# Performance work log

Measured on AMD Instinct MI355X. Metric: run time of the kernel, lower is better.

The kernel has to match this reference:

```python
import jax, jax.numpy as jnp
import numpy as np

E = 512   # embed_size
H = 8     # heads
D = E // H
WIN = 256 # window_size
N = 4     # batch
S = 2048  # seq len (query_len == key_len == value_len)


def setup_inputs() -> dict:
    key = jax.random.key(0)
    ks = jax.random.split(key, 8)
    s = 0.02
    inp = {
        "value": jax.random.normal(ks[0], (N, S, E), jnp.float32),
        "key":   jax.random.normal(ks[1], (N, S, E), jnp.float32),
        "query": jax.random.normal(ks[2], (N, S, E), jnp.float32),
        "mask":  jnp.ones((N, 1, 1, S), jnp.int32),
        # nn.Linear params: y = x @ W.T + b, W shape [out, in]
        "Wv": jax.random.normal(ks[3], (E, E), jnp.float32) * s,
        "bv": jnp.zeros((E,), jnp.float32),
        "Wk": jax.random.normal(ks[4], (E, E), jnp.float32) * s,
        "bk": jnp.zeros((E,), jnp.float32),
        "Wq": jax.random.normal(ks[5], (E, E), jnp.float32) * s,
        "bq": jnp.zeros((E,), jnp.float32),
        "Wo": jax.random.normal(ks[6], (E, E), jnp.float32) * s,
        "bo": jnp.zeros((E,), jnp.float32),
    }
    return inp


def reference(value, key, query, mask, Wv, bv, Wk, bk, Wq, bq, Wo, bo):
    n, q_len, _ = query.shape
    k_len = key.shape[1]
    w = min(WIN, k_len)  # window_size = min(self.window_size, key_len)

    v = (value @ Wv.T + bv).reshape(n, k_len, H, D)
    k = (key   @ Wk.T + bk).reshape(n, k_len, H, D)
    q = (query @ Wq.T + bq).reshape(n, q_len, H, D)

    # Full QK scores; banded window selected below. Position j is inside the
    # window of query i iff  i - w//2 <= j <= i + w//2 (matches the torch
    # per-i slice [max(0,i-w//2), min(k_len, i+w//2+1)) ).
    scores = jnp.einsum('nqhd,nkhd->nhqk', q, k)  # [N,H,Q,K]
    ii = jnp.arange(q_len)[:, None]
    jj = jnp.arange(k_len)[None, :]
    in_win = (jj >= ii - w // 2) & (jj <= ii + w // 2)  # [Q,K]

    # Inside window: scores, masked to -inf where mask == 0.
    # Outside window: entries stay 0 (the torch code zero-inits attention).
    neg_inf = jnp.float32(-jnp.inf)
    banded = jnp.where(mask != 0, scores, neg_inf)          # broadcast [N,1,1,K]
    att_logits = jnp.where(in_win[None, None], banded, 0.0)  # [N,H,Q,K]

    att_logits = att_logits / jnp.sqrt(jnp.float32(E))  # scale by sqrt(embed_size)
    attention = jax.nn.softmax(att_logits, axis=3)

    out = jnp.einsum('nhqk,nkhd->nqhd', attention, v).reshape(n, q_len, E)
    out = out @ Wo.T + bo
    return (out, attention)
```

## Files before the change

### kernel.cpp

```cpp
#include <hip/hip_runtime.h>


typedef unsigned short u16;
typedef __bf16 bf16x8 __attribute__((ext_vector_type(8)));
typedef float  f32x4  __attribute__((ext_vector_type(4)));
typedef u16    u16x8  __attribute__((ext_vector_type(8)));

#define GLOAD_LDS(gsrc, ldst)                                                  \
    __builtin_amdgcn_global_load_lds(                                          \
        (const __attribute__((address_space(1))) void*)(gsrc),                 \
        (__attribute__((address_space(3))) void*)(ldst), 16, 0, 0)

__device__ __forceinline__ u16 f2bf(float f) {
    union { float f; unsigned u; } x; x.f = f;
    unsigned u = x.u;
    u += 0x7fffu + ((u >> 16) & 1u);
    return (u16)(u >> 16);
}
__device__ __forceinline__ int swzc(int c, int r) {
    return (c < 32) ? (c ^ (r & 7)) : c;
}

struct CvtArgs {
    const float* src[7];
    u16*         dst[7];
};

__global__ __launch_bounds__(256) void cvt_kernel(CvtArgs a) {
    int bid = blockIdx.x;
    int t, blk;
    if (bid < 12288) { t = bid >> 12; blk = bid & 4095; }
    else { int r = bid - 12288; t = 3 + (r >> 8); blk = r & 255; }
    int i = (blk * 256 + threadIdx.x) * 4;
    float4 v = *(const float4*)(a.src[t] + i);
    ushort4 o;
    o.x = f2bf(v.x); o.y = f2bf(v.y); o.z = f2bf(v.z); o.w = f2bf(v.w);
    *(ushort4*)(a.dst[t] + i) = o;
}

__global__ __launch_bounds__(256) void gemm_qkv(
    const u16* __restrict__ A0, const u16* __restrict__ A1, const u16* __restrict__ A2,
    const u16* __restrict__ B,
    const float* __restrict__ b0, const float* __restrict__ b1, const float* __restrict__ b2,
    u16* __restrict__ o0, u16* __restrict__ o1, u16* __restrict__ o2,
    float* __restrict__ sumv)
{
    __shared__ __attribute__((aligned(16))) u16 As[128 * 64];
    __shared__ __attribute__((aligned(16))) u16 Bs[128 * 64];

    const int tid  = threadIdx.x;
    const int lane = tid & 63;
    const int w    = tid >> 6;
    const int bm   = blockIdx.x, bn = blockIdx.y;
    const int wm   = w >> 1, wn = w & 1;

    const int t = bn >> 2;
    const u16* A = (t == 0) ? A0 : (t == 1) ? A1 : A2;
    const u16* Ag = A + (size_t)bm * 128 * 512;
    const u16* Bg = B + (size_t)bn * 128 * 512;

    f32x4 acc[4][4];
#pragma unroll
    for (int m = 0; m < 4; ++m)
#pragma unroll
        for (int n = 0; n < 4; ++n) acc[m][n] = 0;

    const int swc = ((lane & 7) ^ (lane >> 3)) * 8;

    for (int k0 = 0; k0 < 512; k0 += 64) {
#pragma unroll
        for (int i = 0; i < 4; ++i) {
            int g = i * 4 + w;
            int row = g * 8 + (lane >> 3);
            GLOAD_LDS(Ag + (size_t)row * 512 + k0 + swc, As + g * 512);
            GLOAD_LDS(Bg + (size_t)row * 512 + k0 + swc, Bs + g * 512);
        }
        __syncthreads();

#pragma unroll
        for (int s = 0; s < 2; ++s) {
            bf16x8 af[4], bf[4];
            int c = s * 4 + (lane >> 4);
#pragma unroll
            for (int m = 0; m < 4; ++m) {
                int r = wm * 64 + m * 16 + (lane & 15);
                af[m] = *(const bf16x8*)(As + r * 64 + ((c ^ (r & 7)) * 8));
                int r2 = wn * 64 + m * 16 + (lane & 15);
                bf[m] = *(const bf16x8*)(Bs + r2 * 64 + ((c ^ (r2 & 7)) * 8));
            }
#pragma unroll
            for (int m = 0; m < 4; ++m)
#pragma unroll
                for (int n = 0; n < 4; ++n)
                    acc[m][n] = __builtin_amdgcn_mfma_f32_16x16x32_bf16(af[m], bf[n], acc[m][n], 0, 0, 0);
        }
        __syncthreads();
    }

    const float* bias = (t == 0) ? b0 : (t == 1) ? b1 : b2;
    u16* ob = (t == 0) ? o0 : (t == 1) ? o1 : o2;
    const int clbase = (bn & 3) * 128;

#pragma unroll
    for (int m = 0; m < 4; ++m) {
#pragma unroll
        for (int n = 0; n < 4; ++n) {
            int cl = clbase + wn * 64 + n * 16 + (lane & 15);
            float bb = bias[cl];
#pragma unroll
            for (int reg = 0; reg < 4; ++reg) {
                int row = bm * 128 + wm * 64 + m * 16 + (lane >> 4) * 4 + reg;
                ob[(size_t)row * 512 + cl] = f2bf(acc[m][n][reg] + bb);
            }
        }
    }

    if (t == 2) {
        int nb = bm >> 4;
#pragma unroll
        for (int n = 0; n < 4; ++n) {
            float s = 0.f;
#pragma unroll
            for (int m = 0; m < 4; ++m)
#pragma unroll
                for (int reg = 0; reg < 4; ++reg) s += acc[m][n][reg];
            s += __shfl_xor(s, 16, 64);
            s += __shfl_xor(s, 32, 64);
            if (lane < 16) {
                int cl = clbase + wn * 64 + n * 16 + lane;
                atomicAdd(sumv + nb * 512 + cl, s);
            }
        }
    }
}

__global__ __launch_bounds__(256) void gemm_o(
    const u16* __restrict__ A, const u16* __restrict__ B,
    const float* __restrict__ bias, float* __restrict__ fo)
{
    __shared__ __attribute__((aligned(16))) u16 As[128 * 64];
    __shared__ __attribute__((aligned(16))) u16 Bs[64 * 64];

    const int tid  = threadIdx.x;
    const int lane = tid & 63;
    const int w    = tid >> 6;
    const int bm   = blockIdx.x, bn = blockIdx.y;
    const int wm   = w >> 1, wn = w & 1;

    const u16* Ag = A + (size_t)bm * 128 * 512;
    const u16* Bg = B + (size_t)bn * 64 * 512;

    f32x4 acc[4][2];
#pragma unroll
    for (int m = 0; m < 4; ++m) { acc[m][0] = 0; acc[m][1] = 0; }

    const int swc = ((lane & 7) ^ (lane >> 3)) * 8;

    for (int k0 = 0; k0 < 512; k0 += 64) {
#pragma unroll
        for (int i = 0; i < 4; ++i) {
            int g = i * 4 + w;
            GLOAD_LDS(Ag + (size_t)(g * 8 + (lane >> 3)) * 512 + k0 + swc, As + g * 512);
        }
#pragma unroll
        for (int i = 0; i < 2; ++i) {
            int g = i * 4 + w;
            GLOAD_LDS(Bg + (size_t)(g * 8 + (lane >> 3)) * 512 + k0 + swc, Bs + g * 512);
        }
        __syncthreads();

#pragma unroll
        for (int s = 0; s < 2; ++s) {
            bf16x8 af[4], bf[2];
            int c = s * 4 + (lane >> 4);
#pragma unroll
            for (int m = 0; m < 4; ++m) {
                int r = wm * 64 + m * 16 + (lane & 15);
                af[m] = *(const bf16x8*)(As + r * 64 + ((c ^ (r & 7)) * 8));
            }
#pragma unroll
            for (int n = 0; n < 2; ++n) {
                int r2 = wn * 32 + n * 16 + (lane & 15);
                bf[n] = *(const bf16x8*)(Bs + r2 * 64 + ((c ^ (r2 & 7)) * 8));
            }
#pragma unroll
            for (int m = 0; m < 4; ++m)
#pragma unroll
                for (int n = 0; n < 2; ++n)
                    acc[m][n] = __builtin_amdgcn_mfma_f32_16x16x32_bf16(af[m], bf[n], acc[m][n], 0, 0, 0);
        }
        __syncthreads();
    }

#pragma unroll
    for (int m = 0; m < 4; ++m) {
#pragma unroll
        for (int n = 0; n < 2; ++n) {
            int cl = bn * 64 + wn * 32 + n * 16 + (lane & 15);
            float bb = bias[cl];
#pragma unroll
            for (int reg = 0; reg < 4; ++reg) {
                int row = bm * 128 + wm * 64 + m * 16 + (lane >> 4) * 4 + reg;
                fo[(size_t)row * 512 + cl] = acc[m][n][reg] + bb;
            }
        }
    }
}

__global__ __launch_bounds__(256) void attn_kernel(
    const u16* __restrict__ qb, const u16* __restrict__ kb,
    const u16* __restrict__ vb, const int* __restrict__ mask,
    const float* __restrict__ sumv, float* __restrict__ att,
    u16* __restrict__ oh, float* __restrict__ c_buf) {
    __shared__ __attribute__((aligned(16))) char lds[78848];
    u16*   Qs      = (u16*)lds;
    float* stat_m  = (float*)lds;
    float* stat_rd = (float*)(lds + 128);
    float* stat_c  = (float*)(lds + 256);
    float* red     = (float*)(lds + 384);
    float* red2    = (float*)(lds + 640);
    u16*   Ks      = (u16*)(lds + 4096);
    u16*   Ab      = Ks;
    u16*   Vt      = (u16*)(lds + 4096 + 36864);

    const int tid  = threadIdx.x;
    const int lane = tid & 63;
    const int w    = tid >> 6;
    const int bid0 = blockIdx.x;
    const int bid  = (bid0 & 7) * 256 + (bid0 >> 3);
    const int tile = bid & 63;
    const int h    = (bid >> 6) & 7;
    const int n    = bid >> 9;
    const int i0   = tile * 32;
    const int jlo  = max(0, i0 - 128);
    const float scale = 0.04419417382415922f;

    const size_t base_nh = (size_t)n * 2048 * 512 + h * 64;
    const int lr = lane >> 3;
    const int swg = ((lane & 7) ^ lr) * 8;

    GLOAD_LDS(qb + base_nh + (size_t)(i0 + w * 8 + lr) * 512 + swg, Qs + w * 512);
    for (int p = 0; p < 9; ++p) {
        int g = p * 4 + w;
        int j = min(jlo + g * 8 + lr, 2047);
        GLOAD_LDS(kb + base_nh + (size_t)j * 512 + swg, Ks + g * 512);
    }
    for (int p = 0; p < 9; ++p) {
        int idx = p * 256 + tid;
        int jj = idx >> 3, ch = idx & 7;
        int j = jlo + jj;
        u16x8 tmp = {0, 0, 0, 0, 0, 0, 0, 0};
        if (j < 2048) tmp = *(const u16x8*)(vb + base_nh + (size_t)j * 512 + ch * 8);
        int jc = jj >> 3, jr = jj & 7;
        int pjc = (jc < 32) ? (jc ^ ch) : jc;
#pragma unroll
        for (int r = 0; r < 8; ++r)
            Vt[(ch * 8 + r) * 296 + pjc * 8 + jr] = tmp[r];
    }
    __syncthreads();

    const int rbase = (w & 1) * 16;
    const int cbase = (w >> 1) * 144;
    f32x4 acc[9];
#pragma unroll
    for (int f = 0; f < 9; ++f) acc[f] = 0;

    bf16x8 aq[2];
    {
        int r = rbase + (lane & 15);
#pragma unroll
        for (int ks = 0; ks < 2; ++ks) {
            int kc = ks * 4 + (lane >> 4);
            aq[ks] = *(const bf16x8*)(Qs + r * 64 + ((kc ^ (r & 7)) * 8));
        }
    }
#pragma unroll
    for (int f = 0; f < 9; ++f) {
        int jj = cbase + f * 16 + (lane & 15);
#pragma unroll
        for (int ks = 0; ks < 2; ++ks) {
            int kc = ks * 4 + (lane >> 4);
            bf16x8 bk_ = *(const bf16x8*)(Ks + jj * 64 + ((kc ^ (jj & 7)) * 8));
            acc[f] = __builtin_amdgcn_mfma_f32_16x16x32_bf16(aq[ks], bk_, acc[f], 0, 0, 0);
        }
    }
    __syncthreads();

    const int rowg = (lane >> 4) * 4;
    f32x4 lv[9];
    float mx[4] = {-__builtin_inff(), -__builtin_inff(), -__builtin_inff(), -__builtin_inff()};
#pragma unroll
    for (int f = 0; f < 9; ++f) {
        int jj = cbase + f * 16 + (lane & 15);
        int j = jlo + jj;
        int mk = (j < 2048) ? mask[n * 2048 + j] : 0;
#pragma unroll
        for (int reg = 0; reg < 4; ++reg) {
            int i = i0 + rbase + rowg + reg;
            bool inw = (j >= i - 128) && (j <= i + 128) && (j < 2048);
            float val = (inw && mk != 0) ? acc[f][reg] * scale : -__builtin_inff();
            lv[f][reg] = val;
            mx[reg] = fmaxf(mx[reg], val);
        }
    }
#pragma unroll
    for (int mskk = 1; mskk < 16; mskk <<= 1)
#pragma unroll
        for (int reg = 0; reg < 4; ++reg)
            mx[reg] = fmaxf(mx[reg], __shfl_xor(mx[reg], mskk, 64));
    if ((lane & 15) == 0) {
#pragma unroll
        for (int reg = 0; reg < 4; ++reg) red[w * 16 + rowg + reg] = mx[reg];
    }
    __syncthreads();
    if (tid < 32) {
        int r = tid;
        int wa = (r < 16) ? 0 : 1, rr = r & 15;
        stat_m[r] = fmaxf(fmaxf(red[wa * 16 + rr], red[(wa + 2) * 16 + rr]), 0.0f);
    }
    __syncthreads();

    float m4[4];
#pragma unroll
    for (int reg = 0; reg < 4; ++reg) m4[reg] = stat_m[rbase + rowg + reg];
    float sm[4] = {0, 0, 0, 0};
#pragma unroll
    for (int f = 0; f < 9; ++f)
#pragma unroll
        for (int reg = 0; reg < 4; ++reg)
            sm[reg] += __expf(lv[f][reg] - m4[reg]);
#pragma unroll
    for (int mskk = 1; mskk < 16; mskk <<= 1)
#pragma unroll
        for (int reg = 0; reg < 4; ++reg)
            sm[reg] += __shfl_xor(sm[reg], mskk, 64);
    if ((lane & 15) == 0) {
#pragma unroll
        for (int reg = 0; reg < 4; ++reg) red2[w * 16 + rowg + reg] = sm[reg];
    }
    __syncthreads();
    if (tid < 32) {
        int r = tid, gi = i0 + r;
        int wa = (r < 16) ? 0 : 1, rr = r & 15;
        float s = red2[wa * 16 + rr] + red2[(wa + 2) * 16 + rr];
        int lo = max(0, gi - 128), hi = min(2048, gi + 129);
        float em = __expf(-stat_m[r]);
        float denom = s + (float)(2048 - (hi - lo)) * em;
        float rd = 1.0f / denom;
        stat_rd[r] = rd;
        float c = em * rd;
        stat_c[r] = c;
        c_buf[(size_t)(n * 8 + h) * 2048 + gi] = c;
    }
    __syncthreads();

    float rd4[4], c4[4];
#pragma unroll
    for (int reg = 0; reg < 4; ++reg) {
        rd4[reg] = stat_rd[rbase + rowg + reg];
        c4[reg] = stat_c[rbase + rowg + reg];
    }
#pragma unroll
    for (int f = 0; f < 9; ++f) {
        int jj = cbase + f * 16 + (lane & 15);
        int j = jlo + jj;
        int jc = jj >> 3;
#pragma unroll
        for (int reg = 0; reg < 4; ++reg) {
            int it = rbase + rowg + reg;
            int i = i0 + it;
            bool inw = (j >= i - 128) && (j <= i + 128) && (j < 2048);
            float e = __expf(lv[f][reg] - m4[reg]);
            float a = inw ? e * rd4[reg] : c4[reg];
            if (j < 2048)
                att[((size_t)(n * 8 + h) * 2048 + i) * 2048 + j] = a;
            float ab = inw ? (a - c4[reg]) : 0.0f;
            ((u16*)((char*)Ab + it * 576 + (swzc(jc, it) << 4)))[jj & 7] = f2bf(ab);
        }
    }
    __syncthreads();

    const int rb2 = (w & 1) * 16;
    const int db  = (w >> 1) * 32;
    f32x4 po[2];
    po[0] = 0; po[1] = 0;
#pragma unroll
    for (int ks = 0; ks < 9; ++ks) {
        int kc = ks * 4 + (lane >> 4);
        int it = rb2 + (lane & 15);
        bf16x8 af = *(const bf16x8*)((char*)Ab + it * 576 + (swzc(kc, it) << 4));
#pragma unroll
        for (int f = 0; f < 2; ++f) {
            int d = db + f * 16 + (lane & 15);
            int phys = (kc < 32) ? (kc ^ (d >> 3)) : kc;
            bf16x8 bv_ = *(const bf16x8*)(Vt + d * 296 + phys * 8);
            po[f] = __builtin_amdgcn_mfma_f32_16x16x32_bf16(af, bv_, po[f], 0, 0, 0);
        }
    }
    {
        const float* svp = sumv + (size_t)n * 512 + h * 64;
#pragma unroll
        for (int f = 0; f < 2; ++f) {
            int d = db + f * 16 + (lane & 15);
            float sv = svp[d];
#pragma unroll
            for (int reg = 0; reg < 4; ++reg) {
                int it = rb2 + rowg + reg;
                float val = po[f][reg] + stat_c[it] * sv;
                oh[base_nh + (size_t)(i0 + it) * 512 + d] = f2bf(val);
            }
        }
    }
}

__global__ __launch_bounds__(256) void fill_kernel(const float* __restrict__ c_buf,
                                                   float* __restrict__ att) {
    __shared__ float cs[32];
    int bid = blockIdx.x;
    int tile = bid & 63, h = (bid >> 6) & 7, n = bid >> 9;
    int i0 = tile * 32;
    int jlo = max(0, i0 - 128);
    int jend = min(2048, jlo + 288);
    int j4lo = jlo >> 2, j4end = jend >> 2;
    int tid = threadIdx.x;
    if (tid < 32) cs[tid] = c_buf[(size_t)(n * 8 + h) * 2048 + i0 + tid];
    __syncthreads();
    size_t rowbase = ((size_t)(n * 8 + h) * 2048 + i0) * 2048;
    for (int idx = tid; idx < 32 * 512; idx += 256) {
        int r = idx >> 9, j4 = idx & 511;
        if (j4 >= j4lo && j4 < j4end) continue;
        float c = cs[r];
        *(float4*)(att + rowbase + (size_t)r * 2048 + j4 * 4) = make_float4(c, c, c, c);
    }
}

extern "C" void kernel_launch(void* const* d_in, const int* in_sizes, int n_in,
                              void* d_out, int out_size, void* d_ws, size_t ws_size,
                              hipStream_t stream) {
    const float* value = (const float*)d_in[0];
    const float* key_  = (const float*)d_in[1];
    const float* query = (const float*)d_in[2];
    const int*   mask  = (const int*)d_in[3];
    const float* Wv = (const float*)d_in[4];
    const float* bv = (const float*)d_in[5];
    const float* Wk = (const float*)d_in[6];
    const float* bk = (const float*)d_in[7];
    const float* Wq = (const float*)d_in[8];
    const float* bq = (const float*)d_in[9];
    const float* Wo = (const float*)d_in[10];
    const float* bo = (const float*)d_in[11];

    char* ws = (char*)d_ws;
    size_t off = 0;
    auto carve = [&](size_t bytes) -> char* {
        char* p = ws + off;
        off += (bytes + 255) & ~(size_t)255;
        return p;
    };
    const size_t XB = (size_t)8192 * 512 * 2;
    const size_t WB = (size_t)512 * 512 * 2;
    u16* xqb  = (u16*)carve(XB);
    u16* xkb  = (u16*)carve(XB);
    u16* xvb  = (u16*)carve(XB);
    u16* wqkv = (u16*)carve(3 * WB);
    u16* wob  = (u16*)carve(WB);
    u16* qb   = (u16*)carve(XB);
    u16* kb   = (u16*)carve(XB);
    u16* vb2  = (u16*)carve(XB);
    u16* ohb  = (u16*)carve(XB);
    float* sumv  = (float*)carve(2048 * sizeof(float));
    float* c_buf = (float*)carve((size_t)65536 * sizeof(float));

    hipMemsetAsync(sumv, 0, 2048 * sizeof(float), stream);

    CvtArgs ca;
    ca.src[0] = query; ca.dst[0] = xqb;
    ca.src[1] = key_;  ca.dst[1] = xkb;
    ca.src[2] = value; ca.dst[2] = xvb;
    ca.src[3] = Wq;    ca.dst[3] = wqkv;
    ca.src[4] = Wk;    ca.dst[4] = wqkv + (size_t)512 * 512;
    ca.src[5] = Wv;    ca.dst[5] = wqkv + (size_t)1024 * 512;
    ca.src[6] = Wo;    ca.dst[6] = wob;

    cvt_kernel<<<dim3(13312), 256, 0, stream>>>(ca);
    gemm_qkv<<<dim3(64, 12), 256, 0, stream>>>(
        xqb, xkb, xvb, wqkv, bq, bk, bv, qb, kb, vb2, sumv);

    float* att = (float*)d_out + (size_t)4 * 2048 * 512;
    attn_kernel<<<dim3(2048), 256, 0, stream>>>(qb, kb, vb2, mask, sumv, att, ohb, c_buf);
    gemm_o<<<dim3(64, 8), 256, 0, stream>>>(ohb, wob, bo, (float*)d_out);
    fill_kernel<<<dim3(2048), 256, 0, stream>>>(c_buf, att);
}
```

Baseline: 670.9 us.

## Fuse activation bf16 conversion into QKV GEMM and fill into attention kernel

The QKV projection GEMM now reads fp32 activations directly and converts them to bf16 in registers before writing them to swizzled LDS. This removes the separate conversion pass and the bf16 activation buffers, and only the weights are still pre-converted. The out-of-window attention fill is moved into the tail of the attention kernel using the in-LDS stat_c values, which drops the c_buf round-trip and one launch. The cost is that the GEMM A-tile load becomes synchronous register loads instead of async global-to-LDS loads, and the attention kernel gets a longer tail of large stores.

Result: no change. 663.4 us (-1.1%).

```diff
diff --git a/kernel.cpp b/kernel.cpp
--- a/kernel.cpp
+++ b/kernel.cpp
@@ -21,16 +21,13 @@
     return (c < 32) ? (c ^ (r & 7)) : c;
 }
 
-struct CvtArgs {
-    const float* src[7];
-    u16*         dst[7];
+struct CvtWArgs {
+    const float* src[4];
+    u16*         dst[4];
 };
 
-__global__ __launch_bounds__(256) void cvt_kernel(CvtArgs a) {
-    int bid = blockIdx.x;
-    int t, blk;
-    if (bid < 12288) { t = bid >> 12; blk = bid & 4095; }
-    else { int r = bid - 12288; t = 3 + (r >> 8); blk = r & 255; }
+__global__ __launch_bounds__(256) void cvt_w(CvtWArgs a) {
+    int t = blockIdx.x >> 8, blk = blockIdx.x & 255;
     int i = (blk * 256 + threadIdx.x) * 4;
     float4 v = *(const float4*)(a.src[t] + i);
     ushort4 o;
@@ -39,7 +36,7 @@
 }
 
 __global__ __launch_bounds__(256) void gemm_qkv(
-    const u16* __restrict__ A0, const u16* __restrict__ A1, const u16* __restrict__ A2,
+    const float* __restrict__ A0, const float* __restrict__ A1, const float* __restrict__ A2,
     const u16* __restrict__ B,
     const float* __restrict__ b0, const float* __restrict__ b1, const float* __restrict__ b2,
     u16* __restrict__ o0, u16* __restrict__ o1, u16* __restrict__ o2,
@@ -55,8 +52,8 @@
     const int wm   = w >> 1, wn = w & 1;
 
     const int t = bn >> 2;
-    const u16* A = (t == 0) ? A0 : (t == 1) ? A1 : A2;
-    const u16* Ag = A + (size_t)bm * 128 * 512;
+    const float* A = (t == 0) ? A0 : (t == 1) ? A1 : A2;
+    const float* Ag = A + (size_t)bm * 128 * 512;
     const u16* Bg = B + (size_t)bn * 128 * 512;
 
     f32x4 acc[4][4];
@@ -66,14 +63,28 @@
         for (int n = 0; n < 4; ++n) acc[m][n] = 0;
 
     const int swc = ((lane & 7) ^ (lane >> 3)) * 8;
+    const int arow = tid >> 1, ahalf = tid & 1;
+    const float* asrc = Ag + (size_t)arow * 512 + ahalf * 32;
 
     for (int k0 = 0; k0 < 512; k0 += 64) {
+        float4 fv[8];
+#pragma unroll
+        for (int i = 0; i < 8; ++i) fv[i] = *(const float4*)(asrc + k0 + i * 4);
+#pragma unroll
+        for (int c4 = 0; c4 < 4; ++c4) {
+            bf16x8 pk;
+#pragma unroll
+            for (int e = 0; e < 8; ++e) {
+                float f = ((const float*)&fv[c4 * 2])[e];
+                pk[e] = (__bf16)f;
+            }
+            int ch = ahalf * 4 + c4;
+            *(bf16x8*)(As + arow * 64 + ((ch ^ (arow & 7)) * 8)) = pk;
+        }
 #pragma unroll
         for (int i = 0; i < 4; ++i) {
             int g = i * 4 + w;
-            int row = g * 8 + (lane >> 3);
-            GLOAD_LDS(Ag + (size_t)row * 512 + k0 + swc, As + g * 512);
-            GLOAD_LDS(Bg + (size_t)row * 512 + k0 + swc, Bs + g * 512);
+            GLOAD_LDS(Bg + (size_t)(g * 8 + (lane >> 3)) * 512 + k0 + swc, Bs + g * 512);
         }
         __syncthreads();
 
@@ -211,7 +222,7 @@
     const u16* __restrict__ qb, const u16* __restrict__ kb,
     const u16* __restrict__ vb, const int* __restrict__ mask,
     const float* __restrict__ sumv, float* __restrict__ att,
-    u16* __restrict__ oh, float* __restrict__ c_buf) {
+    u16* __restrict__ oh) {
     __shared__ __attribute__((aligned(16))) char lds[78848];
     u16*   Qs      = (u16*)lds;
     float* stat_m  = (float*)lds;
@@ -348,9 +359,7 @@
         float denom = s + (float)(2048 - (hi - lo)) * em;
         float rd = 1.0f / denom;
         stat_rd[r] = rd;
-        float c = em * rd;
-        stat_c[r] = c;
-        c_buf[(size_t)(n * 8 + h) * 2048 + gi] = c;
+        stat_c[r] = em * rd;
     }
     __syncthreads();
 
@@ -411,26 +420,17 @@
             }
         }
     }
-}
-
-__global__ __launch_bounds__(256) void fill_kernel(const float* __restrict__ c_buf,
-                                                   float* __restrict__ att) {
-    __shared__ float cs[32];
-    int bid = blockIdx.x;
-    int tile = bid & 63, h = (bid >> 6) & 7, n = bid >> 9;
-    int i0 = tile * 32;
-    int jlo = max(0, i0 - 128);
-    int jend = min(2048, jlo + 288);
-    int j4lo = jlo >> 2, j4end = jend >> 2;
-    int tid = threadIdx.x;
-    if (tid < 32) cs[tid] = c_buf[(size_t)(n * 8 + h) * 2048 + i0 + tid];
-    __syncthreads();
-    size_t rowbase = ((size_t)(n * 8 + h) * 2048 + i0) * 2048;
-    for (int idx = tid; idx < 32 * 512; idx += 256) {
-        int r = idx >> 9, j4 = idx & 511;
-        if (j4 >= j4lo && j4 < j4end) continue;
-        float c = cs[r];
-        *(float4*)(att + rowbase + (size_t)r * 2048 + j4 * 4) = make_float4(c, c, c, c);
+
+    {
+        int jend = min(2048, jlo + 288);
+        int j4lo = jlo >> 2, j4end = jend >> 2;
+        size_t rowbase = ((size_t)(n * 8 + h) * 2048 + i0) * 2048;
+        for (int idx = tid; idx < 32 * 512; idx += 256) {
+            int r = idx >> 9, j4 = idx & 511;
+            if (j4 >= j4lo && j4 < j4end) continue;
+            float c = stat_c[r];
+            *(float4*)(att + rowbase + (size_t)r * 2048 + j4 * 4) = make_float4(c, c, c, c);
+        }
     }
 }
 
@@ -459,35 +459,27 @@
     };
     const size_t XB = (size_t)8192 * 512 * 2;
     const size_t WB = (size_t)512 * 512 * 2;
-    u16* xqb  = (u16*)carve(XB);
-    u16* xkb  = (u16*)carve(XB);
-    u16* xvb  = (u16*)carve(XB);
     u16* wqkv = (u16*)carve(3 * WB);
     u16* wob  = (u16*)carve(WB);
     u16* qb   = (u16*)carve(XB);
     u16* kb   = (u16*)carve(XB);
     u16* vb2  = (u16*)carve(XB);
     u16* ohb  = (u16*)carve(XB);
-    float* sumv  = (float*)carve(2048 * sizeof(float));
-    float* c_buf = (float*)carve((size_t)65536 * sizeof(float));
+    float* sumv = (float*)carve(2048 * sizeof(float));
 
     hipMemsetAsync(sumv, 0, 2048 * sizeof(float), stream);
 
-    CvtArgs ca;
-    ca.src[0] = query; ca.dst[0] = xqb;
-    ca.src[1] = key_;  ca.dst[1] = xkb;
-    ca.src[2] = value; ca.dst[2] = xvb;
-    ca.src[3] = Wq;    ca.dst[3] = wqkv;
-    ca.src[4] = Wk;    ca.dst[4] = wqkv + (size_t)512 * 512;
-    ca.src[5] = Wv;    ca.dst[5] = wqkv + (size_t)1024 * 512;
-    ca.src[6] = Wo;    ca.dst[6] = wob;
-
-    cvt_kernel<<<dim3(13312), 256, 0, stream>>>(ca);
+    CvtWArgs ca;
+    ca.src[0] = Wq; ca.dst[0] = wqkv;
+    ca.src[1] = Wk; ca.dst[1] = wqkv + (size_t)512 * 512;
+    ca.src[2] = Wv; ca.dst[2] = wqkv + (size_t)1024 * 512;
+    ca.src[3] = Wo; ca.dst[3] = wob;
+
+    cvt_w<<<dim3(1024), 256, 0, stream>>>(ca);
     gemm_qkv<<<dim3(64, 12), 256, 0, stream>>>(
-        xqb, xkb, xvb, wqkv, bq, bk, bv, qb, kb, vb2, sumv);
+        query, key_, value, wqkv, bq, bk, bv, qb, kb, vb2, sumv);
 
     float* att = (float*)d_out + (size_t)4 * 2048 * 512;
-    attn_kernel<<<dim3(2048), 256, 0, stream>>>(qb, kb, vb2, mask, sumv, att, ohb, c_buf);
+    attn_kernel<<<dim3(2048), 256, 0, stream>>>(qb, kb, vb2, mask, sumv, att, ohb);
     gemm_o<<<dim3(64, 8), 256, 0, stream>>>(ohb, wob, bo, (float*)d_out);
-    fill_kernel<<<dim3(2048), 256, 0, stream>>>(c_buf, att);
-}
+}
```
